# Optimization experiments

Measured on AMD Instinct MI355X. Metric: run time of the kernel, lower is better.

The kernel has to match this reference:

```python
import jax, jax.numpy as jnp
import numpy as np

EPS = 1e-5


def setup_inputs() -> dict:
    key = jax.random.key(0)
    k0, k1, k2, k3 = jax.random.split(key, 4)
    B, C, H, W = 64, 128, 64, 64
    x = jax.random.normal(k0, (B, C, H, W), dtype=jnp.float32)
    w = jax.random.normal(k1, (C, C, 1), dtype=jnp.float32) * 0.05  # conv1d kernel_size=1 weight
    b = jax.random.normal(k2, (C,), dtype=jnp.float32) * 0.05       # conv1d bias
    s = jax.random.normal(k3, (1, C, 1), dtype=jnp.float32)         # learned per-channel gate logits
    offset = jnp.ones((1,), dtype=jnp.float32) * 8.0                 # module inits offset to 8
    return {"x": x, "w": w, "b": b, "s": s, "offset": offset}


def reference(x, w, b, s, offset):
    B, C, H, W = x.shape
    HW = H * W
    # Checkerboard mask: mask[c, l] = (c + l) % 2  (even channel -> [0,1,0,1,...])
    c_idx = jnp.arange(C)
    l_idx = jnp.arange(HW)
    mask = ((c_idx[:, None] + l_idx[None, :]) % 2).astype(x.dtype)  # (C, HW)

    x_flat = x.reshape(B, C, HW)
    x_masked = x_flat * mask                                         # (B, C, HW)
    # 1x1 conv1d: pointwise channel mix + bias
    z = jnp.einsum('oc,bcl->bol', w[:, :, 0], x_masked) + b[None, :, None]
    pool = z.mean(axis=1)                                            # avgpool over channels -> (B, HW)
    g = jax.nn.sigmoid(pool + offset) + EPS                          # (B, HW)
    s_sig = jax.nn.sigmoid(s[0, :, 0]) + EPS                         # (C,)

    attn_mask = (1.0 - mask)[None] * g[:, None, :] + mask[None] * s_sig[None, :, None]  # (B,C,HW)
    out = x * attn_mask.reshape(B, C, H, W)

    logdet = (C // 2) * jnp.sum(jnp.log(g), axis=-1)                 # (B,)
    logdet = logdet + B * jnp.sum(jnp.log(s_sig)[:, None] * mask)    # scalar broadcast over batch
    return out, logdet
```

## Files before the change

### kernel.cpp

```cpp
#include <hip/hip_runtime.h>
#include <hip/hip_bf16.h>
#include <math.h>


#define EPS 1e-5f
#define NC 128
#define NHW 4096
#define NB 64
#define LT 64
#define NLT (NHW / LT)

typedef __attribute__((ext_vector_type(4))) float f4;


__global__ __launch_bounds__(256) void prep_kernel(const float* __restrict__ w,
                                                   const float* __restrict__ bias,
                                                   const float* __restrict__ s,
                                                   float* __restrict__ ws) {
    __shared__ float wred[8][NC];
    __shared__ float lw[4], bw[4];

    const int tid = threadIdx.x;
    const int q   = tid & 31;
    const int r   = tid >> 5;

    {
        const float* __restrict__ wp = w + (size_t)(r * 16) * NC + q * 4;
        float4 a = make_float4(0.f, 0.f, 0.f, 0.f);
#pragma unroll
        for (int o = 0; o < 16; ++o) {
            const float4 v = *reinterpret_cast<const float4*>(wp + (size_t)o * NC);
            a.x += v.x; a.y += v.y; a.z += v.z; a.w += v.w;
        }
        *reinterpret_cast<float4*>(&wred[r][q * 4]) = a;
    }
    __syncthreads();

    float lv = 0.f, bv = 0.f;
    if (tid < NC) {
        float sum = 0.f;
#pragma unroll
        for (int rr = 0; rr < 8; ++rr) sum += wred[rr][tid];
        ws[tid] = sum * (1.f / NC);
        const float ssig = 1.f / (1.f + __expf(-s[tid])) + EPS;
        ws[NC + tid] = ssig;
        lv = __logf(ssig);
        bv = bias[tid];
    }
#pragma unroll
    for (int off = 32; off > 0; off >>= 1) {
        lv += __shfl_down(lv, off);
        bv += __shfl_down(bv, off);
    }
    const int wave = tid >> 6;
    if ((tid & 63) == 0) { lw[wave] = lv; bw[wave] = bv; }
    __syncthreads();
    if (tid == 0) {
        const float sl = lw[0] + lw[1] + lw[2] + lw[3];
        const float sb = bw[0] + bw[1] + bw[2] + bw[3];
        ws[256] = sb * (1.f / NC);
        ws[257] = (float)NB * (float)(NHW / 2) * sl;
    }
}

__global__ __launch_bounds__(256) void main_kernel(const float* __restrict__ x,
                                                   const float* __restrict__ ws,
                                                   const float* __restrict__ offp,
                                                   float* __restrict__ out,
                                                   float* __restrict__ partials) {
    __shared__ float4 pp[4][16];

    const int tid  = threadIdx.x;
    const int j    = tid & 15;
    const int cg   = tid >> 4;
    const int wave = tid >> 6;
    const int lane = tid & 63;

    const int lt = blockIdx.x;
    const int b  = blockIdx.y;
    const int l0 = lt * LT;

    const size_t base = (size_t)b * (NC * NHW) + (size_t)(cg * 8) * NHW + l0 + j * 4;
    const float* __restrict__ xp = x + base;

    float4 v[8];
#pragma unroll
    for (int k = 0; k < 8; ++k)
        v[k] = *reinterpret_cast<const float4*>(xp + (size_t)k * NHW);

    float4 acc = make_float4(0.f, 0.f, 0.f, 0.f);
#pragma unroll
    for (int k = 0; k < 8; ++k) {
        const int c = cg * 8 + k;
        const float wb = ws[c];
        if (c & 1) { acc.x += wb * v[k].x; acc.z += wb * v[k].z; }
        else       { acc.y += wb * v[k].y; acc.w += wb * v[k].w; }
    }

#pragma unroll
    for (int off = 16; off <= 32; off <<= 1) {
        acc.x += __shfl_xor(acc.x, off);
        acc.y += __shfl_xor(acc.y, off);
        acc.z += __shfl_xor(acc.z, off);
        acc.w += __shfl_xor(acc.w, off);
    }
    if (lane < 16) pp[wave][j] = acc;
    __syncthreads();

    const float4 p0 = pp[0][j], p1 = pp[1][j], p2 = pp[2][j], p3 = pp[3][j];
    const float cst = ws[256] + offp[0];
    float4 g;
    g.x = 1.f / (1.f + __expf(-(p0.x + p1.x + p2.x + p3.x + cst))) + EPS;
    g.y = 1.f / (1.f + __expf(-(p0.y + p1.y + p2.y + p3.y + cst))) + EPS;
    g.z = 1.f / (1.f + __expf(-(p0.z + p1.z + p2.z + p3.z + cst))) + EPS;
    g.w = 1.f / (1.f + __expf(-(p0.w + p1.w + p2.w + p3.w + cst))) + EPS;

    if (wave == 0) {
        float slg = (lane < 16)
                  ? (__logf(g.x) + __logf(g.y) + __logf(g.z) + __logf(g.w))
                  : 0.f;
#pragma unroll
        for (int off = 32; off > 0; off >>= 1) slg += __shfl_down(slg, off);
        if (lane == 0) partials[b * gridDim.x + lt] = slg;
    }

    const float* __restrict__ ssig = ws + NC;
    float* __restrict__ op = out + base;
#pragma unroll
    for (int k = 0; k < 8; ++k) {
        const int c = cg * 8 + k;
        const float sc = ssig[c];
        f4 o;
        if (c & 1) { o.x = v[k].x * sc;  o.y = v[k].y * g.y;
                     o.z = v[k].z * sc;  o.w = v[k].w * g.w; }
        else       { o.x = v[k].x * g.x; o.y = v[k].y * sc;
                     o.z = v[k].z * g.z; o.w = v[k].w * sc; }
        __builtin_nontemporal_store(o, reinterpret_cast<f4*>(op + (size_t)k * NHW));
    }
}

__global__ __launch_bounds__(64) void fin_kernel(const float* __restrict__ partials,
                                                 const float* __restrict__ ws,
                                                 float* __restrict__ logdet,
                                                 int nlt) {
    const int b = blockIdx.x;
    const int t = threadIdx.x;
    float v = (t < nlt) ? partials[b * nlt + t] : 0.f;
#pragma unroll
    for (int off = 32; off > 0; off >>= 1) v += __shfl_down(v, off);
    if (t == 0) logdet[b] = 64.f * v + ws[257];
}

extern "C" void kernel_launch(void* const* d_in, const int* in_sizes, int n_in,
                              void* d_out, int out_size, void* d_ws, size_t ws_size,
                              hipStream_t stream) {
    const float* x    = (const float*)d_in[0];
    const float* w    = (const float*)d_in[1];
    const float* bias = (const float*)d_in[2];
    const float* s    = (const float*)d_in[3];
    const float* offp = (const float*)d_in[4];

    float* out    = (float*)d_out;
    float* logdet = out + (size_t)NB * NC * NHW;
    float* ws     = (float*)d_ws;
    float* partials = ws + 512;

    prep_kernel<<<1, 256, 0, stream>>>(w, bias, s, ws);
    main_kernel<<<dim3(NLT, NB), 256, 0, stream>>>(x, ws, offp, out, partials);
    fin_kernel<<<NB, 64, 0, stream>>>(partials, ws, logdet, NLT);
}
```

Measured before the change: 51.07 us.

## Make each wave own all channels for its columns, removing LDS reduction and barrier

Each wave now covers 16 spatial columns across all 128 channels (16 channel groups by 4 column quads), so the channel-pool reduction finishes entirely with in-wave shuffles. This removes the shared-memory partial buffer and the block-wide __syncthreads, and every wave computes its own gate and writes its own logdet partial. The finalize kernel sums four times as many partials. Per-thread loads are now 16-byte chunks at a 64-byte span per row, which changes coalescing: each row read is 64 contiguous bytes instead of 256.

```diff
diff --git a/kernel.cpp b/kernel.cpp
--- a/kernel.cpp
+++ b/kernel.cpp
@@ -9,6 +9,7 @@
 #define NB 64
 #define LT 64
 #define NLT (NHW / LT)
+#define NPART (NLT * 4)
 
 typedef __attribute__((ext_vector_type(4))) float f4;
 
@@ -68,19 +69,17 @@
                                                    const float* __restrict__ offp,
                                                    float* __restrict__ out,
                                                    float* __restrict__ partials) {
-    __shared__ float4 pp[4][16];
-
     const int tid  = threadIdx.x;
-    const int j    = tid & 15;
-    const int cg   = tid >> 4;
+    const int lane = tid & 63;
     const int wave = tid >> 6;
-    const int lane = tid & 63;
+    const int jq   = lane & 3;
+    const int cg   = lane >> 2;
 
     const int lt = blockIdx.x;
     const int b  = blockIdx.y;
-    const int l0 = lt * LT;
+    const int l0 = lt * LT + wave * 16;
 
-    const size_t base = (size_t)b * (NC * NHW) + (size_t)(cg * 8) * NHW + l0 + j * 4;
+    const size_t base = (size_t)b * (NC * NHW) + (size_t)(cg * 8) * NHW + l0 + jq * 4;
     const float* __restrict__ xp = x + base;
 
     float4 v[8];
@@ -98,30 +97,27 @@
     }
 
 #pragma unroll
-    for (int off = 16; off <= 32; off <<= 1) {
+    for (int off = 4; off <= 32; off <<= 1) {
         acc.x += __shfl_xor(acc.x, off);
         acc.y += __shfl_xor(acc.y, off);
         acc.z += __shfl_xor(acc.z, off);
         acc.w += __shfl_xor(acc.w, off);
     }
-    if (lane < 16) pp[wave][j] = acc;
-    __syncthreads();
 
-    const float4 p0 = pp[0][j], p1 = pp[1][j], p2 = pp[2][j], p3 = pp[3][j];
     const float cst = ws[256] + offp[0];
     float4 g;
-    g.x = 1.f / (1.f + __expf(-(p0.x + p1.x + p2.x + p3.x + cst))) + EPS;
-    g.y = 1.f / (1.f + __expf(-(p0.y + p1.y + p2.y + p3.y + cst))) + EPS;
-    g.z = 1.f / (1.f + __expf(-(p0.z + p1.z + p2.z + p3.z + cst))) + EPS;
-    g.w = 1.f / (1.f + __expf(-(p0.w + p1.w + p2.w + p3.w + cst))) + EPS;
+    g.x = 1.f / (1.f + __expf(-(acc.x + cst))) + EPS;
+    g.y = 1.f / (1.f + __expf(-(acc.y + cst))) + EPS;
+    g.z = 1.f / (1.f + __expf(-(acc.z + cst))) + EPS;
+    g.w = 1.f / (1.f + __expf(-(acc.w + cst))) + EPS;
 
-    if (wave == 0) {
-        float slg = (lane < 16)
+    {
+        float slg = (lane < 4)
                   ? (__logf(g.x) + __logf(g.y) + __logf(g.z) + __logf(g.w))
                   : 0.f;
-#pragma unroll
-        for (int off = 32; off > 0; off >>= 1) slg += __shfl_down(slg, off);
-        if (lane == 0) partials[b * gridDim.x + lt] = slg;
+        slg += __shfl_down(slg, 2);
+        slg += __shfl_down(slg, 1);
+        if (lane == 0) partials[b * NPART + lt * 4 + wave] = slg;
     }
 
     const float* __restrict__ ssig = ws + NC;
@@ -141,11 +137,11 @@
 
 __global__ __launch_bounds__(64) void fin_kernel(const float* __restrict__ partials,
                                                  const float* __restrict__ ws,
-                                                 float* __restrict__ logdet,
-                                                 int nlt) {
+                                                 float* __restrict__ logdet) {
     const int b = blockIdx.x;
     const int t = threadIdx.x;
-    float v = (t < nlt) ? partials[b * nlt + t] : 0.f;
+    const float* __restrict__ pb = partials + b * NPART;
+    float v = pb[t] + pb[t + 64] + pb[t + 128] + pb[t + 192];
 #pragma unroll
     for (int off = 32; off > 0; off >>= 1) v += __shfl_down(v, off);
     if (t == 0) logdet[b] = 64.f * v + ws[257];
@@ -167,5 +163,5 @@
 
     prep_kernel<<<1, 256, 0, stream>>>(w, bias, s, ws);
     main_kernel<<<dim3(NLT, NB), 256, 0, stream>>>(x, ws, offp, out, partials);
-    fin_kernel<<<NB, 64, 0, stream>>>(partials, ws, logdet, NLT);
+    fin_kernel<<<NB, 64, 0, stream>>>(partials, ws, logdet);
 }
```

After: 60.87 us. 19.2% more time.
